# Optimization experiments

Measured on AMD Instinct MI355X. Metric: run time of the kernel, lower is better.

## Reference

```python
import jax, jax.numpy as jnp
import numpy as np

B_, H_, W_ = 4, 64, 64
D_INNER, D_STATE, DT_RANK, K = 192, 16, 6, 4
DT_MIN, DT_MAX = 0.001, 0.1


def setup_inputs() -> dict:
    key = jax.random.key(0)
    ks = jax.random.split(key, 8)
    x = jax.random.normal(ks[0], (B_, D_INNER, H_, W_), dtype=jnp.float32)
    y = jax.random.normal(ks[1], (B_, D_INNER, H_, W_), dtype=jnp.float32)
    # x_proj: 4 stacked Linear(d_inner1 -> dt_rank + 2*d_state) weights
    x_proj_weight = jax.random.normal(ks[2], (K, DT_RANK + 2 * D_STATE, D_INNER), dtype=jnp.float32) * (D_INNER ** -0.5)
    # dt_proj weights: uniform(-dt_rank^-0.5, dt_rank^-0.5)
    s = DT_RANK ** -0.5
    dt_projs_weight = jax.random.uniform(ks[3], (K, D_INNER, DT_RANK), dtype=jnp.float32, minval=-s, maxval=s)
    # dt bias init: inverse softplus of dt ~ loguniform(dt_min, dt_max)
    dt = jnp.exp(jax.random.uniform(ks[4], (K, D_INNER), dtype=jnp.float32)
                 * (np.log(DT_MAX) - np.log(DT_MIN)) + np.log(DT_MIN))
    dt = jnp.clip(dt, 1e-4, None)
    dt_projs_bias = dt + jnp.log(-jnp.expm1(-dt))
    # A_logs: log(1..N) repeated over K*d_inner channels
    A_logs = jnp.tile(jnp.log(jnp.arange(1, D_STATE + 1, dtype=jnp.float32))[None, :], (K * D_INNER, 1))
    Ds = jnp.ones((K * D_INNER,), dtype=jnp.float32)
    ln_gamma = jnp.ones((D_INNER,), dtype=jnp.float32)
    ln_beta = jnp.zeros((D_INNER,), dtype=jnp.float32)
    return {"x": x, "y": y, "x_proj_weight": x_proj_weight, "dt_projs_weight": dt_projs_weight,
            "dt_projs_bias": dt_projs_bias, "A_logs": A_logs, "Ds": Ds,
            "ln_gamma": ln_gamma, "ln_beta": ln_beta}


def _cross_scan(t):
    # (B, C, H, W) -> (B, 4, C, L): [row-major, col-major, and their reverses]
    B, C, H, W = t.shape
    a = t.reshape(B, C, H * W)
    b = jnp.swapaxes(t, 2, 3).reshape(B, C, H * W)
    s = jnp.stack([a, b], axis=1)  # (B,2,C,L)
    return jnp.concatenate([s, jnp.flip(s, axis=-1)], axis=1)  # (B,4,C,L)


def reference(x, y, x_proj_weight, dt_projs_weight, dt_projs_bias, A_logs, Ds, ln_gamma, ln_beta):
    B, C, H, W = x.shape
    L = H * W
    N = A_logs.shape[-1]
    R = dt_projs_weight.shape[-1]
    D = dt_projs_weight.shape[1]

    xs = _cross_scan(x)  # (B,K,C,L)
    ys = _cross_scan(y)  # (B,K,D,L) -- u for the scan

    x_dbl = jnp.einsum('bkdl,kcd->bkcl', xs, x_proj_weight)
    dts, Bs, Cs = x_dbl[:, :, :R], x_dbl[:, :, R:R + N], x_dbl[:, :, R + N:]
    dts = jnp.einsum('bkrl,kdr->bkdl', dts, dt_projs_weight)  # (B,K,D,L)

    delta = jax.nn.softplus(dts + dt_projs_bias.reshape(1, K, D, 1))  # (B,K,D,L)
    A = -jnp.exp(A_logs).reshape(K, D, N)  # (K,D,N)

    # selective scan over L: h_t = exp(delta_t*A)*h_{t-1} + delta_t*B_t*u_t; y_t = C_t . h_t
    u_l = jnp.moveaxis(ys, 3, 0)      # (L,B,K,D)
    d_l = jnp.moveaxis(delta, 3, 0)   # (L,B,K,D)
    B_l = jnp.moveaxis(Bs, 3, 0)      # (L,B,K,N)
    C_l = jnp.moveaxis(Cs, 3, 0)      # (L,B,K,N)

    def step(h, inp):
        u_t, d_t, b_t, c_t = inp
        dA = jnp.exp(d_t[..., None] * A)                       # (B,K,D,N)
        h = dA * h + (d_t * u_t)[..., None] * b_t[:, :, None, :]
        y_t = jnp.einsum('bkdn,bkn->bkd', h, c_t)
        return h, y_t

    h0 = jnp.zeros((B, K, D, N), dtype=jnp.float32)
    _, y_scan = jax.lax.scan(step, h0, (u_l, d_l, B_l, C_l))   # (L,B,K,D)
    out_y = jnp.moveaxis(y_scan, 0, 3) + Ds.reshape(1, K, D, 1) * ys  # (B,K,D,L)

    # cross-merge
    inv_y = jnp.flip(out_y[:, 2:4], axis=-1)                   # (B,2,D,L)
    wh_y = jnp.swapaxes(out_y[:, 1].reshape(B, D, W, H), 2, 3).reshape(B, D, L)
    invwh_y = jnp.swapaxes(inv_y[:, 1].reshape(B, D, W, H), 2, 3).reshape(B, D, L)
    ya = out_y[:, 0] + inv_y[:, 0] + wh_y + invwh_y            # (B,D,L)

    ya = jnp.swapaxes(ya, 1, 2).reshape(B, H, W, D)
    mu = jnp.mean(ya, axis=-1, keepdims=True)
    var = jnp.var(ya, axis=-1, keepdims=True)
    return (ya - mu) * jax.lax.rsqrt(var + 1e-5) * ln_gamma + ln_beta
```

## Files before the change

kernel.cpp:

```cpp
#include <hip/hip_runtime.h>
#include <hip/hip_bf16.h>

#define BB 4
#define KK 4
#define DD 192
#define NN 16
#define RR 6
#define LL 4096
#define NC 64
#define CL 64
#define C38 38

__device__ __forceinline__ float ex2(float x) {
#if __has_builtin(__builtin_amdgcn_exp2f)
  return __builtin_amdgcn_exp2f(x);
#else
  return exp2f(x);
#endif
}

__device__ __forceinline__ int tmap(int k, int tile, int i) {
  if (k == 0 || k == 2) return tile * 64 + i;
  if (k == 1) return i * 64 + tile;
  return 4095 - (i * 64 + tile);
}

__global__ __launch_bounds__(256) void k_proj(
    const float* __restrict__ x, const float* __restrict__ y,
    const float* __restrict__ xpw, const float* __restrict__ dpw,
    const float* __restrict__ dpb,
    float* __restrict__ delta_ws, float* __restrict__ u_ws,
    float* __restrict__ bs_ws, float* __restrict__ cs_ws)
{
  __shared__ float xs[64 * 65];
  __shared__ float xd[38 * 65];
  const int bid = blockIdx.x;
  const int tile = bid & 63;
  const int k = (bid >> 6) & 3;
  const int b = bid >> 8;
  const int tid = threadIdx.x;
  const int ti = tid & 63;
  const int ds4 = tid >> 6;
  const int wv = __builtin_amdgcn_readfirstlane(ds4);

  const int m = (k == 2) ? (4095 - tile * 64 - ti) : (tile * 64 + ti);
  const int tg = tmap(k, tile, ti);
  const size_t bkL = (size_t)(b * KK + k) * LL;

  const int c0 = (wv == 3) ? 28 : wv * 10;
  const float* Wk = xpw + (size_t)k * C38 * DD;
  const float* xb = x + (size_t)b * DD * LL;
  float acc[10];
#pragma unroll
  for (int j = 0; j < 10; ++j) acc[j] = 0.f;

  for (int ch = 0; ch < 3; ++ch) {
    for (int r = ds4; r < 64; r += 4)
      xs[r * 65 + ti] = xb[(size_t)(ch * 64 + r) * LL + m];
    __syncthreads();
    const float* Wc = Wk + ch * 64;
#pragma unroll 8
    for (int dj = 0; dj < 64; ++dj) {
      float xv = xs[dj * 65 + ti];
#pragma unroll
      for (int j = 0; j < 10; ++j)
        acc[j] = fmaf(xv, Wc[(c0 + j) * DD + dj], acc[j]);
    }
    __syncthreads();
  }
#pragma unroll
  for (int j = 0; j < 10; ++j) xd[(c0 + j) * 65 + ti] = acc[j];
  __syncthreads();

  const float* dpwk = dpw + (size_t)k * DD * RR + (size_t)(wv * 48) * RR;
  const float* dpbk = dpb + (size_t)k * DD + wv * 48;
  float* dst = delta_ws + (bkL + tg) * DD + wv * 48;
  for (int j0 = 0; j0 < 48; j0 += 4) {
    float4 v;
    float* vp = (float*)&v;
#pragma unroll
    for (int q = 0; q < 4; ++q) {
      int jj = j0 + q;
      float s = dpbk[jj];
#pragma unroll
      for (int r = 0; r < RR; ++r)
        s = fmaf(xd[r * 65 + ti], dpwk[jj * RR + r], s);
      vp[q] = (s > 20.f) ? s : __logf(1.f + __expf(s));
    }
    *(float4*)(dst + j0) = v;
  }

  for (int idx = tid; idx < 64 * NN; idx += 256) {
    int i = idx >> 4, n = idx & 15;
    int tg2 = tmap(k, tile, i);
    bs_ws[(bkL + tg2) * NN + n] = xd[(RR + n) * 65 + i];
    cs_ws[(bkL + tg2) * NN + n] = xd[(RR + NN + n) * 65 + i];
  }

  const float* yb = y + (size_t)b * DD * LL;
  __syncthreads();
  for (int ch = 0; ch < 3; ++ch) {
    for (int r = ds4; r < 64; r += 4)
      xs[r * 65 + ti] = yb[(size_t)(ch * 64 + r) * LL + m];
    __syncthreads();
    float* udst = u_ws + (bkL + tg) * DD + ch * 64 + wv * 16;
#pragma unroll
    for (int j0 = 0; j0 < 16; j0 += 4) {
      float4 v;
      float* vp = (float*)&v;
#pragma unroll
      for (int q = 0; q < 4; ++q)
        vp[q] = xs[(wv * 16 + j0 + q) * 65 + ti];
      *(float4*)(udst + j0) = v;
    }
    __syncthreads();
  }
}

__global__ __launch_bounds__(192) void k_scan1(
    const float* __restrict__ delta_ws, const float* __restrict__ u_ws,
    const float* __restrict__ bs_ws, const float* __restrict__ A_logs,
    float* __restrict__ cP, float* __restrict__ cS)
{
  __shared__ float Bl[CL * NN];
  const int bid = blockIdx.x;
  const int c = bid & (NC - 1);
  const int bk = bid >> 6;
  const int k = bk & 3;
  const int d = threadIdx.x;
  if (c == NC - 1) return;
  const int t0 = c * CL;

  float A2[NN];
  const float* al = A_logs + (size_t)(k * DD + d) * NN;
#pragma unroll
  for (int n = 0; n < NN; ++n) A2[n] = -__expf(al[n]) * 1.4426950408889634f;

  const float* bsrc = bs_ws + ((size_t)bk * LL + t0) * NN;
  for (int i = threadIdx.x; i < CL * NN; i += 192) Bl[i] = bsrc[i];
  __syncthreads();

  const float* dptr = delta_ws + ((size_t)bk * LL + t0) * DD + d;
  const float* uptr = u_ws + ((size_t)bk * LL + t0) * DD + d;
  float h[NN];
#pragma unroll
  for (int n = 0; n < NN; ++n) h[n] = 0.f;
  float dsum = 0.f;
  float de0 = dptr[0], uu0 = uptr[0];
  float de1 = dptr[DD], uu1 = uptr[DD];
#pragma unroll 2
  for (int t = 0; t < CL; ++t) {
    float de2 = dptr[(t + 2) * DD];
    float uu2 = uptr[(t + 2) * DD];
    float du = de0 * uu0;
    dsum += de0;
    const float4* bq = (const float4*)(Bl + t * NN);
    float4 b0 = bq[0], b1 = bq[1], b2 = bq[2], b3 = bq[3];
    const float bb[16] = {b0.x,b0.y,b0.z,b0.w, b1.x,b1.y,b1.z,b1.w,
                          b2.x,b2.y,b2.z,b2.w, b3.x,b3.y,b3.z,b3.w};
#pragma unroll
    for (int n = 0; n < NN; ++n)
      h[n] = fmaf(ex2(de0 * A2[n]), h[n], du * bb[n]);
    de0 = de1; uu0 = uu1; de1 = de2; uu1 = uu2;
  }
  float* pp = cP + (((size_t)bk * NC + c) * DD + d) * NN;
  float* sp = cS + (((size_t)bk * NC + c) * DD + d) * NN;
#pragma unroll
  for (int n = 0; n < NN; ++n) { pp[n] = ex2(dsum * A2[n]); sp[n] = h[n]; }
}

__global__ __launch_bounds__(256) void k_prefix(
    float* __restrict__ cP, const float* __restrict__ cS)
{
  const int tidg = blockIdx.x * 256 + threadIdx.x;
  const int bk = tidg / (DD * NN);
  const int e = tidg - bk * (DD * NN);
  const size_t base = (size_t)bk * NC * DD * NN + e;
  const int STRIDE = DD * NN;
  float h = 0.f;
  int c = 0;
  for (; c + 4 <= 63; c += 4) {
    float p0 = cP[base + (size_t)(c + 0) * STRIDE];
    float p1 = cP[base + (size_t)(c + 1) * STRIDE];
    float p2 = cP[base + (size_t)(c + 2) * STRIDE];
    float p3 = cP[base + (size_t)(c + 3) * STRIDE];
    float s0 = cS[base + (size_t)(c + 0) * STRIDE];
    float s1 = cS[base + (size_t)(c + 1) * STRIDE];
    float s2 = cS[base + (size_t)(c + 2) * STRIDE];
    float s3 = cS[base + (size_t)(c + 3) * STRIDE];
    h = fmaf(p0, h, s0); cP[base + (size_t)(c + 0) * STRIDE] = h;
    h = fmaf(p1, h, s1); cP[base + (size_t)(c + 1) * STRIDE] = h;
    h = fmaf(p2, h, s2); cP[base + (size_t)(c + 2) * STRIDE] = h;
    h = fmaf(p3, h, s3); cP[base + (size_t)(c + 3) * STRIDE] = h;
  }
  for (; c < 63; ++c) {
    float p = cP[base + (size_t)c * STRIDE];
    float s = cS[base + (size_t)c * STRIDE];
    h = fmaf(p, h, s);
    cP[base + (size_t)c * STRIDE] = h;
  }
}

__global__ __launch_bounds__(192) void k_scan2(
    float* __restrict__ dy_ws,
    const float* __restrict__ u_ws,
    const float* __restrict__ bs_ws, const float* __restrict__ cs_ws,
    const float* __restrict__ A_logs, const float* __restrict__ Ds,
    const float* __restrict__ cHin)
{
  __shared__ float Bl[CL * NN];
  __shared__ float Cl2[CL * NN];
  const int bid = blockIdx.x;
  const int c = bid & (NC - 1);
  const int bk = bid >> 6;
  const int k = bk & 3;
  const int d = threadIdx.x;
  const int t0 = c * CL;

  float A2[NN];
  const float* al = A_logs + (size_t)(k * DD + d) * NN;
#pragma unroll
  for (int n = 0; n < NN; ++n) A2[n] = -__expf(al[n]) * 1.4426950408889634f;
  const float Dkd = Ds[k * DD + d];

  float h[NN];
  if (c == 0) {
#pragma unroll
    for (int n = 0; n < NN; ++n) h[n] = 0.f;
  } else {
    const float4* hq = (const float4*)(cHin + (((size_t)bk * NC + (c - 1)) * DD + d) * NN);
    float4 h0 = hq[0], h1 = hq[1], h2 = hq[2], h3 = hq[3];
    h[0]=h0.x; h[1]=h0.y; h[2]=h0.z; h[3]=h0.w;
    h[4]=h1.x; h[5]=h1.y; h[6]=h1.z; h[7]=h1.w;
    h[8]=h2.x; h[9]=h2.y; h[10]=h2.z; h[11]=h2.w;
    h[12]=h3.x; h[13]=h3.y; h[14]=h3.z; h[15]=h3.w;
  }

  const float* bsrc = bs_ws + ((size_t)bk * LL + t0) * NN;
  const float* csrc = cs_ws + ((size_t)bk * LL + t0) * NN;
  for (int i = threadIdx.x; i < CL * NN; i += 192) {
    Bl[i] = bsrc[i];
    Cl2[i] = csrc[i];
  }
  __syncthreads();

  float* dyp = dy_ws + ((size_t)bk * LL + t0) * DD + d;
  const float* uptr = u_ws + ((size_t)bk * LL + t0) * DD + d;
  float de0 = dyp[0], uu0 = uptr[0];
  float de1 = dyp[DD], uu1 = uptr[DD];
#pragma unroll 2
  for (int t = 0; t < CL; ++t) {
    float de2 = dyp[(t + 2) * DD];
    float uu2 = uptr[(t + 2) * DD];
    float du = de0 * uu0;
    const float4* bq = (const float4*)(Bl + t * NN);
    const float4* cq = (const float4*)(Cl2 + t * NN);
    float4 b0 = bq[0], b1 = bq[1], b2 = bq[2], b3 = bq[3];
    float4 c0 = cq[0], c1 = cq[1], c2 = cq[2], c3 = cq[3];
    const float bb[16] = {b0.x,b0.y,b0.z,b0.w, b1.x,b1.y,b1.z,b1.w,
                          b2.x,b2.y,b2.z,b2.w, b3.x,b3.y,b3.z,b3.w};
    const float cc[16] = {c0.x,c0.y,c0.z,c0.w, c1.x,c1.y,c1.z,c1.w,
                          c2.x,c2.y,c2.z,c2.w, c3.x,c3.y,c3.z,c3.w};
    float yv = 0.f;
#pragma unroll
    for (int n = 0; n < NN; ++n) {
      h[n] = fmaf(ex2(de0 * A2[n]), h[n], du * bb[n]);
      yv = fmaf(h[n], cc[n], yv);
    }
    dyp[t * DD] = fmaf(Dkd, uu0, yv);
    de0 = de1; uu0 = uu1; de1 = de2; uu1 = uu2;
  }
}

__global__ __launch_bounds__(256) void k_comb(
    const float* __restrict__ ybuf, const float* __restrict__ gamma,
    const float* __restrict__ beta, float* __restrict__ out)
{
  const int lane = threadIdx.x & 63;
  const int gl = blockIdx.x * 4 + (threadIdx.x >> 6);
  const int b = gl >> 12;
  const int l = gl & 4095;
  const int hh = l >> 6, ww = l & 63;
  const int lt = ww * 64 + hh;
  const size_t base = (size_t)b * KK * LL * DD;
  const float* y0 = ybuf + base + (size_t)(0 * LL + l) * DD;
  const float* y1 = ybuf + base + (size_t)(1 * LL + lt) * DD;
  const float* y2 = ybuf + base + (size_t)(2 * LL + (4095 - l)) * DD;
  const float* y3 = ybuf + base + (size_t)(3 * LL + (4095 - lt)) * DD;

  float s[3];
  float sum = 0.f, sq = 0.f;
#pragma unroll
  for (int j = 0; j < 3; ++j) {
    int d = lane + j * 64;
    float v = y0[d] + y1[d] + y2[d] + y3[d];
    s[j] = v; sum += v; sq = fmaf(v, v, sq);
  }
#pragma unroll
  for (int o = 1; o < 64; o <<= 1) {
    sum += __shfl_xor(sum, o, 64);
    sq  += __shfl_xor(sq, o, 64);
  }
  const float mu = sum * (1.f / 192.f);
  const float var = sq * (1.f / 192.f) - mu * mu;
  const float inv = rsqrtf(var + 1e-5f);
  float* op = out + (size_t)gl * DD;
#pragma unroll
  for (int j = 0; j < 3; ++j) {
    int d = lane + j * 64;
    op[d] = (s[j] - mu) * inv * gamma[d] + beta[d];
  }
}

extern "C" void kernel_launch(void* const* d_in, const int* in_sizes, int n_in,
                              void* d_out, int out_size, void* d_ws, size_t ws_size,
                              hipStream_t stream) {
  const float* x     = (const float*)d_in[0];
  const float* y     = (const float*)d_in[1];
  const float* xpw   = (const float*)d_in[2];
  const float* dpw   = (const float*)d_in[3];
  const float* dpb   = (const float*)d_in[4];
  const float* alogs = (const float*)d_in[5];
  const float* ds    = (const float*)d_in[6];
  const float* gamma = (const float*)d_in[7];
  const float* beta  = (const float*)d_in[8];
  float* w = (float*)d_ws;

  float* delta = w;
  float* u     = w + 12582912;
  float* bs    = w + 25165824;
  float* cs    = w + 26214400;
  float* cP    = w + 27262976;
  float* cS    = w + 30408704;

  k_proj<<<1024, 256, 0, stream>>>(x, y, xpw, dpw, dpb, delta, u, bs, cs);
  k_scan1<<<1024, 192, 0, stream>>>(delta, u, bs, alogs, cP, cS);
  k_prefix<<<192, 256, 0, stream>>>(cP, cS);
  k_scan2<<<1024, 192, 0, stream>>>(delta, u, bs, cs, alogs, ds, cP);
  k_comb<<<4096, 256, 0, stream>>>(delta, gamma, beta, (float*)d_out);
}
```

Measured before the change: 255.6 us.

## Pre-transpose inputs, halve u workspace, and use smaller scan chunks

Adds a transpose kernel that writes x and y in column-major spatial order into the cP scratch region. The projection kernel can then read the column-scan directions contiguously, and it writes B, C and delta in scan order rather than scattered. The u buffer is now stored only for the two forward directions, and the reverse directions read it with a negative stride, which halves u writes. Scan chunks shrink from 64 to 32 steps with twice as many blocks, raising parallelism at the cost of a longer prefix chain and an extra kernel launch.

Result: slower. 263.8 us (+3.2%).

```diff
diff --git a/kernel.cpp b/kernel.cpp
--- a/kernel.cpp
+++ b/kernel.cpp
@@ -7,8 +7,8 @@
 #define NN 16
 #define RR 6
 #define LL 4096
-#define NC 64
-#define CL 64
+#define NC 128
+#define CL 32
 #define C38 38
 
 __device__ __forceinline__ float ex2(float x) {
@@ -19,14 +19,35 @@
 #endif
 }
 
-__device__ __forceinline__ int tmap(int k, int tile, int i) {
-  if (k == 0 || k == 2) return tile * 64 + i;
-  if (k == 1) return i * 64 + tile;
-  return 4095 - (i * 64 + tile);
+__global__ __launch_bounds__(256) void k_trans(
+    const float* __restrict__ x, const float* __restrict__ y,
+    float* __restrict__ xT, float* __restrict__ yT)
+{
+  __shared__ float t0l[64 * 65];
+  __shared__ float t1l[64 * 65];
+  const int tid = threadIdx.x;
+  const int ti = tid & 63;
+  const int r4 = tid >> 6;
+  const int mm0 = blockIdx.x * 2;
+  const int mm1 = mm0 + 1;
+  const float* s0 = (mm0 < 768 ? x + (size_t)mm0 * 4096 : y + (size_t)(mm0 - 768) * 4096);
+  const float* s1 = (mm1 < 768 ? x + (size_t)mm1 * 4096 : y + (size_t)(mm1 - 768) * 4096);
+  float* d0 = (mm0 < 768 ? xT + (size_t)mm0 * 4096 : yT + (size_t)(mm0 - 768) * 4096);
+  float* d1 = (mm1 < 768 ? xT + (size_t)mm1 * 4096 : yT + (size_t)(mm1 - 768) * 4096);
+#pragma unroll
+  for (int r = r4; r < 64; r += 4) t0l[r * 65 + ti] = s0[r * 64 + ti];
+#pragma unroll
+  for (int r = r4; r < 64; r += 4) t1l[r * 65 + ti] = s1[r * 64 + ti];
+  __syncthreads();
+#pragma unroll
+  for (int r = r4; r < 64; r += 4) d0[r * 64 + ti] = t0l[ti * 65 + r];
+#pragma unroll
+  for (int r = r4; r < 64; r += 4) d1[r * 64 + ti] = t1l[ti * 65 + r];
 }
 
 __global__ __launch_bounds__(256) void k_proj(
     const float* __restrict__ x, const float* __restrict__ y,
+    const float* __restrict__ xT, const float* __restrict__ yT,
     const float* __restrict__ xpw, const float* __restrict__ dpw,
     const float* __restrict__ dpb,
     float* __restrict__ delta_ws, float* __restrict__ u_ws,
@@ -43,13 +64,14 @@
   const int ds4 = tid >> 6;
   const int wv = __builtin_amdgcn_readfirstlane(ds4);
 
-  const int m = (k == 2) ? (4095 - tile * 64 - ti) : (tile * 64 + ti);
-  const int tg = tmap(k, tile, ti);
+  const int m = (k >= 2) ? (4095 - tile * 64 - ti) : (tile * 64 + ti);
+  const int tg = tile * 64 + ti;
   const size_t bkL = (size_t)(b * KK + k) * LL;
+
+  const float* xb = ((k & 1) ? xT : x) + (size_t)b * DD * LL;
 
   const int c0 = (wv == 3) ? 28 : wv * 10;
   const float* Wk = xpw + (size_t)k * C38 * DD;
-  const float* xb = x + (size_t)b * DD * LL;
   float acc[10];
 #pragma unroll
   for (int j = 0; j < 10; ++j) acc[j] = 0.f;
@@ -92,28 +114,31 @@
 
   for (int idx = tid; idx < 64 * NN; idx += 256) {
     int i = idx >> 4, n = idx & 15;
-    int tg2 = tmap(k, tile, i);
-    bs_ws[(bkL + tg2) * NN + n] = xd[(RR + n) * 65 + i];
-    cs_ws[(bkL + tg2) * NN + n] = xd[(RR + NN + n) * 65 + i];
-  }
-
-  const float* yb = y + (size_t)b * DD * LL;
-  __syncthreads();
-  for (int ch = 0; ch < 3; ++ch) {
-    for (int r = ds4; r < 64; r += 4)
-      xs[r * 65 + ti] = yb[(size_t)(ch * 64 + r) * LL + m];
+    size_t row = bkL + tile * 64 + i;
+    bs_ws[row * NN + n] = xd[(RR + n) * 65 + i];
+    cs_ws[row * NN + n] = xd[(RR + NN + n) * 65 + i];
+  }
+
+  if (k < 2) {
+    const float* yb = ((k & 1) ? yT : y) + (size_t)b * DD * LL;
+    const size_t ubkL = (size_t)(b * 2 + k) * LL;
     __syncthreads();
-    float* udst = u_ws + (bkL + tg) * DD + ch * 64 + wv * 16;
-#pragma unroll
-    for (int j0 = 0; j0 < 16; j0 += 4) {
-      float4 v;
-      float* vp = (float*)&v;
-#pragma unroll
-      for (int q = 0; q < 4; ++q)
-        vp[q] = xs[(wv * 16 + j0 + q) * 65 + ti];
-      *(float4*)(udst + j0) = v;
+    for (int ch = 0; ch < 3; ++ch) {
+      for (int r = ds4; r < 64; r += 4)
+        xs[r * 65 + ti] = yb[(size_t)(ch * 64 + r) * LL + m];
+      __syncthreads();
+      float* udst = u_ws + (ubkL + tg) * DD + ch * 64 + wv * 16;
+#pragma unroll
+      for (int j0 = 0; j0 < 16; j0 += 4) {
+        float4 v;
+        float* vp = (float*)&v;
+#pragma unroll
+        for (int q = 0; q < 4; ++q)
+          vp[q] = xs[(wv * 16 + j0 + q) * 65 + ti];
+        *(float4*)(udst + j0) = v;
+      }
+      __syncthreads();
     }
-    __syncthreads();
   }
 }
 
@@ -125,8 +150,9 @@
   __shared__ float Bl[CL * NN];
   const int bid = blockIdx.x;
   const int c = bid & (NC - 1);
-  const int bk = bid >> 6;
+  const int bk = bid >> 7;
   const int k = bk & 3;
+  const int b = bk >> 2;
   const int d = threadIdx.x;
   if (c == NC - 1) return;
   const int t0 = c * CL;
@@ -141,17 +167,21 @@
   __syncthreads();
 
   const float* dptr = delta_ws + ((size_t)bk * LL + t0) * DD + d;
-  const float* uptr = u_ws + ((size_t)bk * LL + t0) * DD + d;
+  const int rev = k >> 1;
+  const float* uptr = u_ws +
+      ((size_t)(b * 2 + (k & 1)) * LL + (rev ? (LL - 1 - t0) : t0)) * DD + d;
+  const int ustep = rev ? -DD : DD;
+
   float h[NN];
 #pragma unroll
   for (int n = 0; n < NN; ++n) h[n] = 0.f;
   float dsum = 0.f;
   float de0 = dptr[0], uu0 = uptr[0];
-  float de1 = dptr[DD], uu1 = uptr[DD];
+  float de1 = dptr[DD], uu1 = uptr[ustep];
 #pragma unroll 2
   for (int t = 0; t < CL; ++t) {
     float de2 = dptr[(t + 2) * DD];
-    float uu2 = uptr[(t + 2) * DD];
+    float uu2 = uptr[(t + 2) * ustep];
     float du = de0 * uu0;
     dsum += de0;
     const float4* bq = (const float4*)(Bl + t * NN);
@@ -179,7 +209,7 @@
   const int STRIDE = DD * NN;
   float h = 0.f;
   int c = 0;
-  for (; c + 4 <= 63; c += 4) {
+  for (; c + 4 <= NC - 1; c += 4) {
     float p0 = cP[base + (size_t)(c + 0) * STRIDE];
     float p1 = cP[base + (size_t)(c + 1) * STRIDE];
     float p2 = cP[base + (size_t)(c + 2) * STRIDE];
@@ -193,7 +223,7 @@
     h = fmaf(p2, h, s2); cP[base + (size_t)(c + 2) * STRIDE] = h;
     h = fmaf(p3, h, s3); cP[base + (size_t)(c + 3) * STRIDE] = h;
   }
-  for (; c < 63; ++c) {
+  for (; c < NC - 1; ++c) {
     float p = cP[base + (size_t)c * STRIDE];
     float s = cS[base + (size_t)c * STRIDE];
     h = fmaf(p, h, s);
@@ -212,8 +242,9 @@
   __shared__ float Cl2[CL * NN];
   const int bid = blockIdx.x;
   const int c = bid & (NC - 1);
-  const int bk = bid >> 6;
+  const int bk = bid >> 7;
   const int k = bk & 3;
+  const int b = bk >> 2;
   const int d = threadIdx.x;
   const int t0 = c * CL;
 
@@ -245,13 +276,17 @@
   __syncthreads();
 
   float* dyp = dy_ws + ((size_t)bk * LL + t0) * DD + d;
-  const float* uptr = u_ws + ((size_t)bk * LL + t0) * DD + d;
+  const int rev = k >> 1;
+  const float* uptr = u_ws +
+      ((size_t)(b * 2 + (k & 1)) * LL + (rev ? (LL - 1 - t0) : t0)) * DD + d;
+  const int ustep = rev ? -DD : DD;
+
   float de0 = dyp[0], uu0 = uptr[0];
-  float de1 = dyp[DD], uu1 = uptr[DD];
+  float de1 = dyp[DD], uu1 = uptr[ustep];
 #pragma unroll 2
   for (int t = 0; t < CL; ++t) {
     float de2 = dyp[(t + 2) * DD];
-    float uu2 = uptr[(t + 2) * DD];
+    float uu2 = uptr[(t + 2) * ustep];
     float du = de0 * uu0;
     const float4* bq = (const float4*)(Bl + t * NN);
     const float4* cq = (const float4*)(Cl2 + t * NN);
@@ -328,14 +363,17 @@
 
   float* delta = w;
   float* u     = w + 12582912;
-  float* bs    = w + 25165824;
-  float* cs    = w + 26214400;
-  float* cP    = w + 27262976;
-  float* cS    = w + 30408704;
-
-  k_proj<<<1024, 256, 0, stream>>>(x, y, xpw, dpw, dpb, delta, u, bs, cs);
-  k_scan1<<<1024, 192, 0, stream>>>(delta, u, bs, alogs, cP, cS);
+  float* bs    = w + 18874368;
+  float* cs    = w + 19922944;
+  float* cP    = w + 20971520;
+  float* cS    = w + 27262976;
+  float* xT    = cP;
+  float* yT    = cP + 3145728;
+
+  k_trans<<<768, 256, 0, stream>>>(x, y, xT, yT);
+  k_proj<<<1024, 256, 0, stream>>>(x, y, xT, yT, xpw, dpw, dpb, delta, u, bs, cs);
+  k_scan1<<<2048, 192, 0, stream>>>(delta, u, bs, alogs, cP, cS);
   k_prefix<<<192, 256, 0, stream>>>(cP, cS);
-  k_scan2<<<1024, 192, 0, stream>>>(delta, u, bs, cs, alogs, ds, cP);
+  k_scan2<<<2048, 192, 0, stream>>>(delta, u, bs, cs, alogs, ds, cP);
   k_comb<<<4096, 256, 0, stream>>>(delta, gamma, beta, (float*)d_out);
 }
```
